# Kernel tuning notes

Measured on AMD Instinct MI355X. Metric: run time of the kernel, lower is better.

Reference implementation:

```python
import jax, jax.numpy as jnp
import numpy as np

B, N, D, K, H = 64, 4096, 256, 15, 512
EPS = 1e-8
LN_EPS = 1e-5

def layer_norm(x, w, b):
    m = jnp.mean(x, axis=-1, keepdims=True)
    v = jnp.mean((x - m) ** 2, axis=-1, keepdims=True)
    return (x - m) / jnp.sqrt(v + LN_EPS) * w + b

def gru_cell(x, h, w_ih, w_hh, b_ih, b_hh):
    gi = x @ w_ih.T + b_ih
    gh = h @ w_hh.T + b_hh
    ir, iz, inn = jnp.split(gi, 3, axis=-1)
    hr, hz, hn = jnp.split(gh, 3, axis=-1)
    r = jax.nn.sigmoid(ir + hr)
    z = jax.nn.sigmoid(iz + hz)
    n = jnp.tanh(inn + r * hn)
    return (1.0 - z) * n + z * h

def setup_inputs() -> dict:
    key = jax.random.key(0)
    ks = jax.random.split(key, 16)
    s = 1.0 / np.sqrt(D)
    return {
        "inputs": jax.random.normal(ks[0], (B, N, D), jnp.float32),
        "slot_noise": jax.random.normal(ks[1], (B, K, D), jnp.float32),
        "slots_mu": jax.random.normal(ks[2], (1, K, D), jnp.float32) * s,
        "slots_logsigma": jnp.zeros((1, K, D), jnp.float32),
        "Wq": jax.random.normal(ks[3], (D, D), jnp.float32) * s,
        "Wk": jax.random.normal(ks[4], (D, D), jnp.float32) * s,
        "Wv": jax.random.normal(ks[5], (D, D), jnp.float32) * s,
        "gru_w_ih": jax.random.normal(ks[6], (3 * D, D), jnp.float32) * s,
        "gru_w_hh": jax.random.normal(ks[7], (3 * D, D), jnp.float32) * s,
        "gru_b_ih": jnp.zeros((3 * D,), jnp.float32),
        "gru_b_hh": jnp.zeros((3 * D,), jnp.float32),
        "mlp_w1": jax.random.normal(ks[8], (H, D), jnp.float32) * s,
        "mlp_b1": jnp.zeros((H,), jnp.float32),
        "mlp_w2": jax.random.normal(ks[9], (D, H), jnp.float32) / np.sqrt(H),
        "mlp_b2": jnp.zeros((D,), jnp.float32),
        "ln_in_w": jnp.ones((D,), jnp.float32), "ln_in_b": jnp.zeros((D,), jnp.float32),
        "ln_slots_w": jnp.ones((D,), jnp.float32), "ln_slots_b": jnp.zeros((D,), jnp.float32),
        "ln_mlp_w": jnp.ones((D,), jnp.float32), "ln_mlp_b": jnp.zeros((D,), jnp.float32),
    }

def reference(inputs, slot_noise, slots_mu, slots_logsigma, Wq, Wk, Wv,
              gru_w_ih, gru_w_hh, gru_b_ih, gru_b_hh,
              mlp_w1, mlp_b1, mlp_w2, mlp_b2,
              ln_in_w, ln_in_b, ln_slots_w, ln_slots_b, ln_mlp_w, ln_mlp_b):
    scale = D ** (-0.5)
    slots = slots_mu + jnp.exp(slots_logsigma) * slot_noise  # (B,K,D)
    x = layer_norm(inputs, ln_in_w, ln_in_b)
    k = x @ Wk.T  # (B,N,D)
    v = x @ Wv.T
    for _ in range(3):
        slots_prev = slots
        s = layer_norm(slots, ln_slots_w, ln_slots_b)
        q = s @ Wq.T  # (B,K,D)
        attn_logits = jnp.einsum('bkd,bnd->bkn', q, k) * scale
        attn = jax.nn.softmax(attn_logits, axis=1)  # softmax over slots
        attn_norm = attn / (jnp.sum(attn, axis=-1, keepdims=True) + EPS)
        updates = jnp.einsum('bkn,bnd->bkd', attn_norm, v)
        slots = gru_cell(updates.reshape(-1, D), slots_prev.reshape(-1, D),
                         gru_w_ih, gru_w_hh, gru_b_ih, gru_b_hh).reshape(B, K, D)
        h1 = jax.nn.relu(layer_norm(slots, ln_mlp_w, ln_mlp_b) @ mlp_w1.T + mlp_b1)
        slots = slots + h1 @ mlp_w2.T + mlp_b2
    s = layer_norm(slots, ln_slots_w, ln_slots_b)
    q = s @ Wq.T
    attn_logits = jnp.einsum('bkd,bnd->bkn', q, k) * scale
    attn = jax.nn.softmax(attn_logits, axis=1)
    return (slots, attn)
```

## Files before the change

### kernel.cpp

```cpp
#include <hip/hip_runtime.h>
#include <hip/hip_bf16.h>
#include <stdint.h>

#define Bh 64
#define Nn 4096
#define Dd 256
#define Kk 15
#define Hh 512
#define BN (Bh*Nn)
#define EPSN 1e-8f
#define LN_EPS 1e-5f

typedef __attribute__((ext_vector_type(8))) short short8;
typedef __attribute__((ext_vector_type(4))) float f32x4;

__device__ __forceinline__ float bflo(unsigned u){ return __uint_as_float(u << 16); }
__device__ __forceinline__ float bfhi(unsigned u){ return __uint_as_float(u & 0xffff0000u); }
__device__ __forceinline__ unsigned short f2bf(float f){
    unsigned b = __float_as_uint(f);
    b += 0x7fffu + ((b >> 16) & 1u);
    return (unsigned short)(b >> 16);
}
__device__ __forceinline__ float sigm_(float x){ return 1.f/(1.f+__expf(-x)); }
__device__ __forceinline__ float tanh_(float x){ return 1.f - 2.f/(__expf(2.f*x)+1.f); }

__device__ __forceinline__ void async16(const void* g, void* l){
    __builtin_amdgcn_global_load_lds((const __attribute__((address_space(1))) void*)g,
                                     (__attribute__((address_space(3))) void*)l, 16, 0, 0);
}

#define OFF_X    ((size_t)0)
#define OFF_K    (OFF_X  + (size_t)BN*256*2)
#define OFF_VT   (OFF_K  + (size_t)BN*256*2)
#define OFF_WC   (OFF_VT + (size_t)BN*256*2)
#define OFF_QBF  (OFF_WC + (size_t)512*256*2)
#define OFF_S    (OFF_QBF+ (size_t)64*16*256*2)
#define OFF_G    (OFF_S  + (size_t)983040)
#define OFF_SN   (OFF_G  + (size_t)983040)
#define OFF_UPD  (OFF_SN + (size_t)983040)
#define OFF_ASUM (OFF_UPD+ (size_t)983040)
#define OFF_GT   (OFF_ASUM+(size_t)4096)
#define OFF_H1   (OFF_GT + (size_t)960*1536*4)

__global__ __launch_bounds__(256) void k_prep_wc(const float* __restrict__ Wk, const float* __restrict__ Wv,
                                                 unsigned short* __restrict__ Wc){
    int i = blockIdx.x*256 + threadIdx.x;
    int n = i >> 8, e = i & 255;
    float w = (n < 256) ? Wk[n*256+e] : Wv[(n-256)*256+e];
    Wc[i] = f2bf(w);
}

__global__ __launch_bounds__(256) void k_slots_init(const float* __restrict__ mu, const float* __restrict__ lsig,
                                                    const float* __restrict__ noise, float* __restrict__ S){
    int i = blockIdx.x*256 + threadIdx.x;
    int j = i % (Kk*Dd);
    S[i] = mu[j] + __expf(lsig[j]) * noise[i];
}

__global__ __launch_bounds__(256) void k_ln_in(const float* __restrict__ x, const float* __restrict__ g,
                                               const float* __restrict__ b, unsigned short* __restrict__ out){
    int wave = threadIdx.x >> 6, lane = threadIdx.x & 63;
    size_t row = (size_t)blockIdx.x*4 + wave;
    const float4* xr = (const float4*)(x + row*Dd);
    float4 v = xr[lane];
    float s  = v.x+v.y+v.z+v.w;
    float ss = v.x*v.x+v.y*v.y+v.z*v.z+v.w*v.w;
    for (int m=1;m<64;m<<=1){ s += __shfl_xor(s,m); ss += __shfl_xor(ss,m); }
    float mean = s*(1.f/Dd);
    float rstd = rsqrtf(ss*(1.f/Dd) - mean*mean + LN_EPS);
    float4 gv = ((const float4*)g)[lane], bv = ((const float4*)b)[lane];
    ushort4 o;
    o.x = f2bf((v.x-mean)*rstd*gv.x + bv.x);
    o.y = f2bf((v.y-mean)*rstd*gv.y + bv.y);
    o.z = f2bf((v.z-mean)*rstd*gv.z + bv.z);
    o.w = f2bf((v.w-mean)*rstd*gv.w + bv.w);
    *(ushort4*)(out + row*Dd + lane*4) = o;
}

__global__ __launch_bounds__(256) void k_ln_rows(const float* __restrict__ x, const float* __restrict__ g,
                                                 const float* __restrict__ b, float* __restrict__ out){
    int wave = threadIdx.x >> 6, lane = threadIdx.x & 63;
    size_t row = (size_t)blockIdx.x*4 + wave;
    const float4* xr = (const float4*)(x + row*Dd);
    float4 v = xr[lane];
    float s  = v.x+v.y+v.z+v.w;
    float ss = v.x*v.x+v.y*v.y+v.z*v.z+v.w*v.w;
    for (int m=1;m<64;m<<=1){ s += __shfl_xor(s,m); ss += __shfl_xor(ss,m); }
    float mean = s*(1.f/Dd);
    float rstd = rsqrtf(ss*(1.f/Dd) - mean*mean + LN_EPS);
    float4 gv = ((const float4*)g)[lane], bv = ((const float4*)b)[lane];
    float4 o;
    o.x = (v.x-mean)*rstd*gv.x + bv.x;
    o.y = (v.y-mean)*rstd*gv.y + bv.y;
    o.z = (v.z-mean)*rstd*gv.z + bv.z;
    o.w = (v.w-mean)*rstd*gv.w + bv.w;
    *(float4*)(out + row*Dd + lane*4) = o;
}

__global__ __launch_bounds__(512, 2) void k_proj(const unsigned short* __restrict__ A,
                                                 const unsigned short* __restrict__ Bw,
                                                 unsigned short* __restrict__ kb,
                                                 unsigned short* __restrict__ vT){
    __shared__ short As[128*256];
    int tid = threadIdx.x;
    int w = tid >> 6, lane = tid & 63;
    int m0 = blockIdx.x*128;
    int wr = w >> 2, wc = w & 3;
    int lr = lane & 15, lg = lane >> 4;

#pragma unroll
    for (int j=0;j<8;j++){
        int idx = j*512 + tid;
        int row = idx >> 5, chp = idx & 31;
        int ch  = chp ^ (row & 7);
        async16((const char*)A + ((size_t)(m0+row)*256 + ch*8)*2, (char*)As + (size_t)idx*16);
    }

    const unsigned short* bwl = Bw + (size_t)(wc*32 + lr)*256 + lg*8;

    short8 A_0,A_1,A_2,A_3, B_0,B_1,B_2,B_3, C_0,C_1,C_2,C_3;
    f32x4 acc00,acc01,acc10,acc11,acc20,acc21,acc30,acc31;

#define ISSUE(P, t_) { \
    const unsigned short* bp_ = bwl + ((t_)>>2)*32768 + (((t_)>>1)&1)*128 + ((t_)&1)*64; \
    P##0 = *(const short8*)(bp_); \
    P##1 = *(const short8*)(bp_ + 32); \
    P##2 = *(const short8*)(bp_ + 4096); \
    P##3 = *(const short8*)(bp_ + 4096 + 32); }
#define LDA(mi_, ks_) (*(const short8*)((const char*)As + (wr*64 + (mi_)*16 + lr)*512 + ((((ks_)*4+lg))^swz)*16))
#define MF(a_,b_,c_) __builtin_amdgcn_mfma_f32_16x16x32_bf16(a_,b_,c_,0,0,0)
#define COMPQ(F0, F1, ks_) { \
    short8 af0=LDA(0,ks_), af1=LDA(1,ks_), af2=LDA(2,ks_), af3=LDA(3,ks_); \
    acc00=MF(af0,F0,acc00); acc01=MF(af0,F1,acc01); \
    acc10=MF(af1,F0,acc10); acc11=MF(af1,F1,acc11); \
    acc20=MF(af2,F0,acc20); acc21=MF(af2,F1,acc21); \
    acc30=MF(af3,F0,acc30); acc31=MF(af3,F1,acc31); }
#define COMPU(P, t_) { COMPQ(P##0, P##2, ((((t_)>>1)&1)*4 + ((t_)&1)*2 + 0)); \
                       COMPQ(P##1, P##3, ((((t_)>>1)&1)*4 + ((t_)&1)*2 + 1)); }
#define ZERO { acc00=acc01=acc10=acc11=acc20=acc21=acc30=acc31=(f32x4){0.f,0.f,0.f,0.f}; }
#define STK(nt_, mi_, ni_, A_) { \
    int gn_ = (nt_)*128 + wc*32 + (ni_)*16 + cn; \
    _Pragma("unroll") for (int r=0;r<4;r++){ \
        size_t gm_ = (size_t)m0 + wr*64 + (mi_)*16 + cr + r; \
        kb[gm_*256 + gn_] = f2bf(A_[r]); } }
#define STV(nt_, mi_, ni_, A_) { \
    int nl_ = nl0 + wr*64 + (mi_)*16 + cr; \
    int d_  = ((nt_)-2)*128 + wc*32 + (ni_)*16 + cn; \
    ushort4 o_; o_.x=f2bf(A_[0]); o_.y=f2bf(A_[1]); o_.z=f2bf(A_[2]); o_.w=f2bf(A_[3]); \
    *(ushort4*)(vT + ((size_t)bb*256 + d_)*4096 + nl_) = o_; }
#define EPI_K(nt_) { STK(nt_,0,0,acc00) STK(nt_,0,1,acc01) STK(nt_,1,0,acc10) STK(nt_,1,1,acc11) \
                     STK(nt_,2,0,acc20) STK(nt_,2,1,acc21) STK(nt_,3,0,acc30) STK(nt_,3,1,acc31) }
#define EPI_V(nt_) { STV(nt_,0,0,acc00) STV(nt_,0,1,acc01) STV(nt_,1,0,acc10) STV(nt_,1,1,acc11) \
                     STV(nt_,2,0,acc20) STV(nt_,2,1,acc21) STV(nt_,3,0,acc30) STV(nt_,3,1,acc31) }

    ISSUE(A_,0) ISSUE(B_,1) ISSUE(C_,2)
    __syncthreads();

    int bb  = m0 >> 12;
    int nl0 = m0 & 4095;
    int cn = lr, cr = lg*4;
    int swz = lr & 7;

    ZERO
    COMPU(A_,0)  ISSUE(A_,3)
    COMPU(B_,1)  ISSUE(B_,4)
    COMPU(C_,2)  ISSUE(C_,5)
    COMPU(A_,3)  ISSUE(A_,6)
    EPI_K(0) ZERO
    COMPU(B_,4)  ISSUE(B_,7)
    COMPU(C_,5)  ISSUE(C_,8)
    COMPU(A_,6)  ISSUE(A_,9)
    COMPU(B_,7)  ISSUE(B_,10)
    EPI_K(1) ZERO
    COMPU(C_,8)  ISSUE(C_,11)
    COMPU(A_,9)  ISSUE(A_,12)
    COMPU(B_,10) ISSUE(B_,13)
    COMPU(C_,11) ISSUE(C_,14)
    EPI_V(2) ZERO
    COMPU(A_,12) ISSUE(A_,15)
    COMPU(B_,13)
    COMPU(C_,14)
    COMPU(A_,15)
    EPI_V(3)

#undef ISSUE
#undef LDA
#undef MF
#undef COMPQ
#undef COMPU
#undef ZERO
#undef STK
#undef STV
#undef EPI_K
#undef EPI_V
}

__global__ __launch_bounds__(256) void k_q(const float* __restrict__ sn, const float* __restrict__ Wq,
                                           unsigned short* __restrict__ qbf){
    int b = blockIdx.x, c = threadIdx.x;
    const float4* wr = (const float4*)(Wq + (size_t)c*256);
    const float4* s4 = (const float4*)(sn + (size_t)b*Kk*Dd);
    float acc[15];
#pragma unroll
    for (int r=0;r<15;r++) acc[r] = 0.f;
    for (int e=0;e<64;e++){
        float4 wv = wr[e];
#pragma unroll
        for (int r=0;r<15;r++){
            float4 sv = s4[r*64+e];
            acc[r] += sv.x*wv.x + sv.y*wv.y + sv.z*wv.z + sv.w*wv.w;
        }
    }
#pragma unroll
    for (int r=0;r<15;r++) qbf[(size_t)b*4096 + r*256 + c] = f2bf(acc[r]);
    qbf[(size_t)b*4096 + 15*256 + c] = 0;
}

__global__ __launch_bounds__(256) void k_attn(const unsigned short* __restrict__ kbuf,
                                              const unsigned short* __restrict__ vT,
                                              const unsigned short* __restrict__ qbf,
                                              float* __restrict__ part, float* __restrict__ asum){
    __shared__ unsigned short qls[16*264];
    __shared__ unsigned short atn[4][16*72];
    __shared__ float asl[16];
    int tid = threadIdx.x;
    int w = tid >> 6, l = tid & 63;
    int b = blockIdx.y, n0 = blockIdx.x*256;
    if (tid < 16) asl[tid] = 0.f;
    {
        const short8* qg = (const short8*)(qbf + (size_t)b*4096);
        for (int i = tid; i < 512; i += 256){
            int row = i >> 5, cc = i & 31;
            *(short8*)&qls[row*264 + cc*8] = qg[i];
        }
    }
    __syncthreads();
    int lr = l & 15, lg = l >> 4;
    f32x4 acc[4];
#pragma unroll
    for (int t=0;t<4;t++) acc[t] = (f32x4){0.f,0.f,0.f,0.f};
    const unsigned short* kb = kbuf + ((size_t)(b*Nn) + n0 + w*64)*256;
#pragma unroll
    for (int ks=0; ks<8; ks++){
        short8 af = *(const short8*)&qls[lr*264 + ks*32 + lg*8];
#pragma unroll
        for (int t=0;t<4;t++){
            short8 bf = *(const short8*)(kb + ((size_t)(t*16+lr))*256 + ks*32 + lg*8);
            acc[t] = __builtin_amdgcn_mfma_f32_16x16x32_bf16(af, bf, acc[t], 0,0,0);
        }
    }
    float asr[4] = {0.f,0.f,0.f,0.f};
#pragma unroll
    for (int t=0;t<4;t++){
        float v0=acc[t][0], v1=acc[t][1], v2=acc[t][2], v3=acc[t][3];
        if (lg==3) v3 = -1e30f;
        float m = fmaxf(fmaxf(v0,v1), fmaxf(v2,v3));
        m = fmaxf(m, __shfl_xor(m,16));
        m = fmaxf(m, __shfl_xor(m,32));
        float e0=__expf((v0-m)*0.0625f), e1=__expf((v1-m)*0.0625f),
              e2=__expf((v2-m)*0.0625f), e3=(lg==3)?0.f:__expf((v3-m)*0.0625f);
        float s = e0+e1+e2+e3;
        s += __shfl_xor(s,16); s += __shfl_xor(s,32);
        float inv = 1.f/s;
        e0*=inv; e1*=inv; e2*=inv; e3*=inv;
        unsigned short* a_ = &atn[w][0];
        int col = t*16 + lr;
        a_[(lg*4+0)*72+col] = f2bf(e0);
        a_[(lg*4+1)*72+col] = f2bf(e1);
        a_[(lg*4+2)*72+col] = f2bf(e2);
        a_[(lg*4+3)*72+col] = f2bf(e3);
        float p0=e0,p1=e1,p2=e2,p3=e3;
        for (int mk=1;mk<16;mk<<=1){
            p0+=__shfl_xor(p0,mk); p1+=__shfl_xor(p1,mk);
            p2+=__shfl_xor(p2,mk); p3+=__shfl_xor(p3,mk);
        }
        asr[0]+=p0; asr[1]+=p1; asr[2]+=p2; asr[3]+=p3;
    }
    if (lr == 0){
        atomicAdd(&asl[lg*4+0], asr[0]);
        atomicAdd(&asl[lg*4+1], asr[1]);
        atomicAdd(&asl[lg*4+2], asr[2]);
        atomicAdd(&asl[lg*4+3], asr[3]);
    }
    __syncthreads();
    f32x4 ua[4];
#pragma unroll
    for (int dt=0;dt<4;dt++) ua[dt] = (f32x4){0.f,0.f,0.f,0.f};
    const unsigned short* vb = vT + (size_t)b*256*4096 + ((size_t)(w*64 + lr))*4096 + n0 + lg*8;
#pragma unroll
    for (int wn=0;wn<4;wn++)
#pragma unroll
        for (int kc=0;kc<2;kc++){
            short8 af = *(const short8*)&atn[wn][lr*72 + kc*32 + lg*8];
#pragma unroll
            for (int dt=0;dt<4;dt++){
                short8 bf = *(const short8*)(vb + (size_t)dt*16*4096 + wn*64 + kc*32);
                ua[dt] = __builtin_amdgcn_mfma_f32_16x16x32_bf16(af, bf, ua[dt], 0,0,0);
            }
        }
    float* pb = part + ((size_t)(b*16 + blockIdx.x))*4096;
#pragma unroll
    for (int dt=0;dt<4;dt++)
#pragma unroll
        for (int r=0;r<4;r++)
            pb[(lg*4+r)*256 + w*64 + dt*16 + lr] = ua[dt][r];
    if (tid < 15) atomicAdd(&asum[b*15+tid], asl[tid]);
}

__global__ __launch_bounds__(256) void k_upd_reduce(const float* __restrict__ part, float* __restrict__ upd){
    int i = blockIdx.x*256 + threadIdx.x;
    int b = i / 3840, rem = i - b*3840;
    const float* p = part + (size_t)b*16*4096 + rem;
    float s = 0.f;
#pragma unroll
    for (int j=0;j<16;j++) s += p[j*4096];
    upd[i] = s;
}

__global__ __launch_bounds__(256) void k_gates(const float* __restrict__ upd, const float* __restrict__ asum,
                                               const float* __restrict__ S,
                                               const float* __restrict__ wih, const float* __restrict__ whh,
                                               const float* __restrict__ bih, const float* __restrict__ bhh,
                                               float* __restrict__ gates){
    int b = blockIdx.y;
    int c = blockIdx.x*256 + threadIdx.x;
    bool isGI = (c < 768);
    const float* wrow = isGI ? (wih + (size_t)c*256) : (whh + (size_t)(c-768)*256);
    const float* src  = isGI ? (upd + (size_t)b*Kk*Dd) : (S + (size_t)b*Kk*Dd);
    float bias = isGI ? bih[c] : bhh[c-768];
    const float4* w4 = (const float4*)wrow;
    const float4* s4 = (const float4*)src;
    float acc[15];
#pragma unroll
    for (int r=0;r<15;r++) acc[r] = 0.f;
    for (int e=0;e<64;e++){
        float4 wv = w4[e];
#pragma unroll
        for (int r=0;r<15;r++){
            float4 sv = s4[r*64+e];
            acc[r] += sv.x*wv.x + sv.y*wv.y + sv.z*wv.z + sv.w*wv.w;
        }
    }
#pragma unroll
    for (int r=0;r<15;r++){
        float v = acc[r];
        if (isGI) v *= 1.f/(asum[b*Kk+r] + EPSN);
        gates[((size_t)(b*Kk+r))*1536 + c] = v + bias;
    }
}

__global__ __launch_bounds__(256) void k_gru(const float* __restrict__ gates, const float* __restrict__ S,
                                             float* __restrict__ G){
    int row = blockIdx.x, d = threadIdx.x;
    const float* gr = gates + (size_t)row*1536;
    float ir=gr[d], iz=gr[256+d], inn=gr[512+d];
    float hr=gr[768+d], hz=gr[1024+d], hn=gr[1280+d];
    float r = sigm_(ir+hr), z = sigm_(iz+hz);
    float n = tanh_(inn + r*hn);
    float h = S[(size_t)row*Dd + d];
    G[(size_t)row*Dd + d] = (1.f-z)*n + z*h;
}

__global__ __launch_bounds__(256) void k_mlp1(const float* __restrict__ sn, const float* __restrict__ w1,
                                              const float* __restrict__ b1, float* __restrict__ h1){
    int b = blockIdx.y;
    int c = blockIdx.x*256 + threadIdx.x;
    const float4* w4 = (const float4*)(w1 + (size_t)c*256);
    const float4* s4 = (const float4*)(sn + (size_t)b*Kk*Dd);
    float acc[15];
#pragma unroll
    for (int r=0;r<15;r++) acc[r] = 0.f;
    for (int e=0;e<64;e++){
        float4 wv = w4[e];
#pragma unroll
        for (int r=0;r<15;r++){
            float4 sv = s4[r*64+e];
            acc[r] += sv.x*wv.x + sv.y*wv.y + sv.z*wv.z + sv.w*wv.w;
        }
    }
    float bias = b1[c];
#pragma unroll
    for (int r=0;r<15;r++)
        h1[((size_t)(b*Kk+r))*Hh + c] = fmaxf(acc[r] + bias, 0.f);
}

__global__ __launch_bounds__(256) void k_mlp2(const float* __restrict__ G, const float* __restrict__ h1,
                                              const float* __restrict__ w2, const float* __restrict__ b2,
                                              float* __restrict__ S){
    int b = blockIdx.x, c = threadIdx.x;
    const float4* w4 = (const float4*)(w2 + (size_t)c*512);
    const float4* h4 = (const float4*)(h1 + (size_t)b*Kk*Hh);
    float acc[15];
#pragma unroll
    for (int r=0;r<15;r++) acc[r] = 0.f;
    for (int e=0;e<128;e++){
        float4 wv = w4[e];
#pragma unroll
        for (int r=0;r<15;r++){
            float4 hv = h4[r*128+e];
            acc[r] += hv.x*wv.x + hv.y*wv.y + hv.z*wv.z + hv.w*wv.w;
        }
    }
    float bias = b2[c];
#pragma unroll
    for (int r=0;r<15;r++){
        size_t i = ((size_t)(b*Kk+r))*Dd + c;
        S[i] = G[i] + acc[r] + bias;
    }
}

__global__ __launch_bounds__(256) void k_attn_out(const unsigned short* __restrict__ kbuf,
                                                  const unsigned short* __restrict__ qbf,
                                                  float* __restrict__ out){
    __shared__ unsigned short qls[16*264];
    int tid = threadIdx.x;
    int w = tid >> 6, l = tid & 63;
    int b = blockIdx.y, n0 = blockIdx.x*256;
    {
        const short8* qg = (const short8*)(qbf + (size_t)b*4096);
        for (int i = tid; i < 512; i += 256){
            int row = i >> 5, cc = i & 31;
            *(short8*)&qls[row*264 + cc*8] = qg[i];
        }
    }
    __syncthreads();
    int lr = l & 15, lg = l >> 4;
    f32x4 acc[4];
#pragma unroll
    for (int t=0;t<4;t++) acc[t] = (f32x4){0.f,0.f,0.f,0.f};
    const unsigned short* kb = kbuf + ((size_t)(b*Nn) + n0 + w*64)*256;
#pragma unroll
    for (int ks=0; ks<8; ks++){
        short8 af = *(const short8*)&qls[lr*264 + ks*32 + lg*8];
#pragma unroll
        for (int t=0;t<4;t++){
            short8 bf = *(const short8*)(kb + ((size_t)(t*16+lr))*256 + ks*32 + lg*8);
            acc[t] = __builtin_amdgcn_mfma_f32_16x16x32_bf16(af, bf, acc[t], 0,0,0);
        }
    }
#pragma unroll
    for (int t=0;t<4;t++){
        float v0=acc[t][0], v1=acc[t][1], v2=acc[t][2], v3=acc[t][3];
        if (lg==3) v3 = -1e30f;
        float m = fmaxf(fmaxf(v0,v1), fmaxf(v2,v3));
        m = fmaxf(m, __shfl_xor(m,16));
        m = fmaxf(m, __shfl_xor(m,32));
        float e0=__expf((v0-m)*0.0625f), e1=__expf((v1-m)*0.0625f),
              e2=__expf((v2-m)*0.0625f), e3=(lg==3)?0.f:__expf((v3-m)*0.0625f);
        float s = e0+e1+e2+e3;
        s += __shfl_xor(s,16); s += __shfl_xor(s,32);
        float inv = 1.f/s;
        int n = n0 + w*64 + t*16 + lr;
        float ee0=e0*inv, ee1=e1*inv, ee2=e2*inv, ee3=e3*inv;
        out[((size_t)(b*15 + lg*4+0))*4096 + n] = ee0;
        out[((size_t)(b*15 + lg*4+1))*4096 + n] = ee1;
        out[((size_t)(b*15 + lg*4+2))*4096 + n] = ee2;
        if (lg != 3) out[((size_t)(b*15 + lg*4+3))*4096 + n] = ee3;
    }
}

__global__ __launch_bounds__(256) void k_copy(const float* __restrict__ src, float* __restrict__ dst){
    int i = blockIdx.x*256 + threadIdx.x;
    dst[i] = src[i];
}

extern "C" void kernel_launch(void* const* d_in, const int* in_sizes, int n_in,
                              void* d_out, int out_size, void* d_ws, size_t ws_size,
                              hipStream_t stream) {
    const float* inputs = (const float*)d_in[0];
    const float* noise  = (const float*)d_in[1];
    const float* mu     = (const float*)d_in[2];
    const float* lsig   = (const float*)d_in[3];
    const float* Wq     = (const float*)d_in[4];
    const float* Wk     = (const float*)d_in[5];
    const float* Wv     = (const float*)d_in[6];
    const float* wih    = (const float*)d_in[7];
    const float* whh    = (const float*)d_in[8];
    const float* bih    = (const float*)d_in[9];
    const float* bhh    = (const float*)d_in[10];
    const float* w1     = (const float*)d_in[11];
    const float* b1     = (const float*)d_in[12];
    const float* w2     = (const float*)d_in[13];
    const float* b2     = (const float*)d_in[14];
    const float* lin_w  = (const float*)d_in[15];
    const float* lin_b  = (const float*)d_in[16];
    const float* lsl_w  = (const float*)d_in[17];
    const float* lsl_b  = (const float*)d_in[18];
    const float* lml_w  = (const float*)d_in[19];
    const float* lml_b  = (const float*)d_in[20];

    char* ws = (char*)d_ws;
    unsigned short* xbf  = (unsigned short*)(ws + OFF_X);
    float*          PART = (float*)(ws + OFF_X);
    unsigned short* kbuf = (unsigned short*)(ws + OFF_K);
    unsigned short* vT   = (unsigned short*)(ws + OFF_VT);
    unsigned short* wc   = (unsigned short*)(ws + OFF_WC);
    unsigned short* QBF  = (unsigned short*)(ws + OFF_QBF);
    float* S    = (float*)(ws + OFF_S);
    float* G    = (float*)(ws + OFF_G);
    float* SN   = (float*)(ws + OFF_SN);
    float* UPD  = (float*)(ws + OFF_UPD);
    float* ASUM = (float*)(ws + OFF_ASUM);
    float* GT   = (float*)(ws + OFF_GT);
    float* H1   = (float*)(ws + OFF_H1);
    float* out  = (float*)d_out;

    k_prep_wc<<<512, 256, 0, stream>>>(Wk, Wv, wc);
    k_slots_init<<<960, 256, 0, stream>>>(mu, lsig, noise, S);
    k_ln_in<<<BN/4, 256, 0, stream>>>(inputs, lin_w, lin_b, xbf);
    k_proj<<<BN/128, 512, 0, stream>>>(xbf, wc, kbuf, vT);

    for (int it = 0; it < 3; it++){
        k_ln_rows<<<240, 256, 0, stream>>>(S, lsl_w, lsl_b, SN);
        k_q<<<Bh, 256, 0, stream>>>(SN, Wq, QBF);
        hipMemsetAsync(ASUM, 0, 4096, stream);
        k_attn<<<dim3(16, Bh), 256, 0, stream>>>(kbuf, vT, QBF, PART, ASUM);
        k_upd_reduce<<<960, 256, 0, stream>>>(PART, UPD);
        k_gates<<<dim3(6, Bh), 256, 0, stream>>>(UPD, ASUM, S, wih, whh, bih, bhh, GT);
        k_gru<<<960, 256, 0, stream>>>(GT, S, G);
        k_ln_rows<<<240, 256, 0, stream>>>(G, lml_w, lml_b, SN);
        k_mlp1<<<dim3(2, Bh), 256, 0, stream>>>(SN, w1, b1, H1);
        k_mlp2<<<Bh, 256, 0, stream>>>(G, H1, w2, b2, S);
    }

    k_ln_rows<<<240, 256, 0, stream>>>(S, lsl_w, lsl_b, SN);
    k_q<<<Bh, 256, 0, stream>>>(SN, Wq, QBF);
    k_attn_out<<<dim3(16, Bh), 256, 0, stream>>>(kbuf, QBF, out + 245760);
    k_copy<<<960, 256, 0, stream>>>(S, out);
}
```

Before: 1.407 ms.

## Fuse layer norms into consumer kernels and fold reductions into gate kernel

Fuses the input layer norm into the K/V projection kernel, which now reads fp32 inputs and writes normalized bf16 rows straight into LDS, so the bf16 x intermediate is never written to or read from global memory. Slot and MLP layer norms move into the q and mlp1 kernels. Attention partial sums and row sums are reduced inside the gates kernel instead of through an atomic memset path and a separate reduce kernel. The final slots are written to the output from mlp2, which removes the copy kernel. The projection kernel loses its async global-to-LDS loads and does more ALU work before the MFMA phase, and each gates block repeats the partial reduction.

```diff
diff --git a/kernel.cpp b/kernel.cpp
--- a/kernel.cpp
+++ b/kernel.cpp
@@ -14,8 +14,6 @@
 typedef __attribute__((ext_vector_type(8))) short short8;
 typedef __attribute__((ext_vector_type(4))) float f32x4;
 
-__device__ __forceinline__ float bflo(unsigned u){ return __uint_as_float(u << 16); }
-__device__ __forceinline__ float bfhi(unsigned u){ return __uint_as_float(u & 0xffff0000u); }
 __device__ __forceinline__ unsigned short f2bf(float f){
     unsigned b = __float_as_uint(f);
     b += 0x7fffu + ((b >> 16) & 1u);
@@ -23,11 +21,6 @@
 }
 __device__ __forceinline__ float sigm_(float x){ return 1.f/(1.f+__expf(-x)); }
 __device__ __forceinline__ float tanh_(float x){ return 1.f - 2.f/(__expf(2.f*x)+1.f); }
-
-__device__ __forceinline__ void async16(const void* g, void* l){
-    __builtin_amdgcn_global_load_lds((const __attribute__((address_space(1))) void*)g,
-                                     (__attribute__((address_space(3))) void*)l, 16, 0, 0);
-}
 
 #define OFF_X    ((size_t)0)
 #define OFF_K    (OFF_X  + (size_t)BN*256*2)
@@ -57,47 +50,9 @@
     S[i] = mu[j] + __expf(lsig[j]) * noise[i];
 }
 
-__global__ __launch_bounds__(256) void k_ln_in(const float* __restrict__ x, const float* __restrict__ g,
-                                               const float* __restrict__ b, unsigned short* __restrict__ out){
-    int wave = threadIdx.x >> 6, lane = threadIdx.x & 63;
-    size_t row = (size_t)blockIdx.x*4 + wave;
-    const float4* xr = (const float4*)(x + row*Dd);
-    float4 v = xr[lane];
-    float s  = v.x+v.y+v.z+v.w;
-    float ss = v.x*v.x+v.y*v.y+v.z*v.z+v.w*v.w;
-    for (int m=1;m<64;m<<=1){ s += __shfl_xor(s,m); ss += __shfl_xor(ss,m); }
-    float mean = s*(1.f/Dd);
-    float rstd = rsqrtf(ss*(1.f/Dd) - mean*mean + LN_EPS);
-    float4 gv = ((const float4*)g)[lane], bv = ((const float4*)b)[lane];
-    ushort4 o;
-    o.x = f2bf((v.x-mean)*rstd*gv.x + bv.x);
-    o.y = f2bf((v.y-mean)*rstd*gv.y + bv.y);
-    o.z = f2bf((v.z-mean)*rstd*gv.z + bv.z);
-    o.w = f2bf((v.w-mean)*rstd*gv.w + bv.w);
-    *(ushort4*)(out + row*Dd + lane*4) = o;
-}
-
-__global__ __launch_bounds__(256) void k_ln_rows(const float* __restrict__ x, const float* __restrict__ g,
-                                                 const float* __restrict__ b, float* __restrict__ out){
-    int wave = threadIdx.x >> 6, lane = threadIdx.x & 63;
-    size_t row = (size_t)blockIdx.x*4 + wave;
-    const float4* xr = (const float4*)(x + row*Dd);
-    float4 v = xr[lane];
-    float s  = v.x+v.y+v.z+v.w;
-    float ss = v.x*v.x+v.y*v.y+v.z*v.z+v.w*v.w;
-    for (int m=1;m<64;m<<=1){ s += __shfl_xor(s,m); ss += __shfl_xor(ss,m); }
-    float mean = s*(1.f/Dd);
-    float rstd = rsqrtf(ss*(1.f/Dd) - mean*mean + LN_EPS);
-    float4 gv = ((const float4*)g)[lane], bv = ((const float4*)b)[lane];
-    float4 o;
-    o.x = (v.x-mean)*rstd*gv.x + bv.x;
-    o.y = (v.y-mean)*rstd*gv.y + bv.y;
-    o.z = (v.z-mean)*rstd*gv.z + bv.z;
-    o.w = (v.w-mean)*rstd*gv.w + bv.w;
-    *(float4*)(out + row*Dd + lane*4) = o;
-}
-
-__global__ __launch_bounds__(512, 2) void k_proj(const unsigned short* __restrict__ A,
+__global__ __launch_bounds__(512, 2) void k_proj(const float* __restrict__ X,
+                                                 const float* __restrict__ lnw,
+                                                 const float* __restrict__ lnb,
                                                  const unsigned short* __restrict__ Bw,
                                                  unsigned short* __restrict__ kb,
                                                  unsigned short* __restrict__ vT){
@@ -108,12 +63,32 @@
     int wr = w >> 2, wc = w & 3;
     int lr = lane & 15, lg = lane >> 4;
 
-#pragma unroll
-    for (int j=0;j<8;j++){
-        int idx = j*512 + tid;
-        int row = idx >> 5, chp = idx & 31;
-        int ch  = chp ^ (row & 7);
-        async16((const char*)A + ((size_t)(m0+row)*256 + ch*8)*2, (char*)As + (size_t)idx*16);
+    {
+        float4 gv = ((const float4*)lnw)[lane];
+        float4 bv = ((const float4*)lnb)[lane];
+        const float* xr0 = X + ((size_t)(m0 + w*16))*256 + lane*4;
+#pragma unroll
+        for (int bt=0; bt<2; bt++){
+            float4 xv[8];
+#pragma unroll
+            for (int r=0;r<8;r++) xv[r] = *(const float4*)(xr0 + (size_t)(bt*8+r)*256);
+#pragma unroll
+            for (int r=0;r<8;r++){
+                float4 v = xv[r];
+                float s  = v.x+v.y+v.z+v.w;
+                float ss = v.x*v.x+v.y*v.y+v.z*v.z+v.w*v.w;
+                for (int mk=1;mk<64;mk<<=1){ s += __shfl_xor(s,mk); ss += __shfl_xor(ss,mk); }
+                float mean = s*(1.f/256.f);
+                float rstd = rsqrtf(ss*(1.f/256.f) - mean*mean + LN_EPS);
+                ushort4 o;
+                o.x = f2bf((v.x-mean)*rstd*gv.x + bv.x);
+                o.y = f2bf((v.y-mean)*rstd*gv.y + bv.y);
+                o.z = f2bf((v.z-mean)*rstd*gv.z + bv.z);
+                o.w = f2bf((v.w-mean)*rstd*gv.w + bv.w);
+                int row = w*16 + bt*8 + r;
+                *(ushort4*)((char*)As + row*512 + (((lane>>1)^(row&7))<<4) + ((lane&1)<<3)) = o;
+            }
+        }
     }
 
     const unsigned short* bwl = Bw + (size_t)(wc*32 + lr)*256 + lg*8;
@@ -195,31 +170,53 @@
 #undef EPI_V
 }
 
-__global__ __launch_bounds__(256) void k_q(const float* __restrict__ sn, const float* __restrict__ Wq,
-                                           unsigned short* __restrict__ qbf){
-    int b = blockIdx.x, c = threadIdx.x;
-    const float4* wr = (const float4*)(Wq + (size_t)c*256);
-    const float4* s4 = (const float4*)(sn + (size_t)b*Kk*Dd);
+__global__ __launch_bounds__(256) void k_lnq(const float* __restrict__ S,
+                                             const float* __restrict__ g, const float* __restrict__ b,
+                                             const float* __restrict__ Wq,
+                                             unsigned short* __restrict__ qbf){
+    __shared__ float sn[15*256];
+    int tid = threadIdx.x, w = tid >> 6, lane = tid & 63;
+    int bb = blockIdx.x;
+    {
+        float4 gv = ((const float4*)g)[lane], bv = ((const float4*)b)[lane];
+        for (int r=w; r<15; r+=4){
+            float4 v = *(const float4*)(S + ((size_t)bb*15 + r)*256 + lane*4);
+            float s  = v.x+v.y+v.z+v.w;
+            float ss = v.x*v.x+v.y*v.y+v.z*v.z+v.w*v.w;
+            for (int mk=1;mk<64;mk<<=1){ s += __shfl_xor(s,mk); ss += __shfl_xor(ss,mk); }
+            float mean = s*(1.f/256.f);
+            float rstd = rsqrtf(ss*(1.f/256.f) - mean*mean + LN_EPS);
+            float4 o;
+            o.x = (v.x-mean)*rstd*gv.x + bv.x;
+            o.y = (v.y-mean)*rstd*gv.y + bv.y;
+            o.z = (v.z-mean)*rstd*gv.z + bv.z;
+            o.w = (v.w-mean)*rstd*gv.w + bv.w;
+            *(float4*)(sn + r*256 + lane*4) = o;
+        }
+    }
+    __syncthreads();
+    int c = tid;
+    const float4* wr4 = (const float4*)(Wq + (size_t)c*256);
     float acc[15];
 #pragma unroll
     for (int r=0;r<15;r++) acc[r] = 0.f;
     for (int e=0;e<64;e++){
-        float4 wv = wr[e];
+        float4 wv = wr4[e];
 #pragma unroll
         for (int r=0;r<15;r++){
-            float4 sv = s4[r*64+e];
+            float4 sv = *(const float4*)(sn + r*256 + e*4);
             acc[r] += sv.x*wv.x + sv.y*wv.y + sv.z*wv.z + sv.w*wv.w;
         }
     }
 #pragma unroll
-    for (int r=0;r<15;r++) qbf[(size_t)b*4096 + r*256 + c] = f2bf(acc[r]);
-    qbf[(size_t)b*4096 + 15*256 + c] = 0;
+    for (int r=0;r<15;r++) qbf[(size_t)bb*4096 + r*256 + c] = f2bf(acc[r]);
+    qbf[(size_t)bb*4096 + 15*256 + c] = 0;
 }
 
 __global__ __launch_bounds__(256) void k_attn(const unsigned short* __restrict__ kbuf,
                                               const unsigned short* __restrict__ vT,
                                               const unsigned short* __restrict__ qbf,
-                                              float* __restrict__ part, float* __restrict__ asum){
+                                              float* __restrict__ part, float* __restrict__ asump){
     __shared__ unsigned short qls[16*264];
     __shared__ unsigned short atn[4][16*72];
     __shared__ float asl[16];
@@ -304,32 +301,45 @@
 #pragma unroll
         for (int r=0;r<4;r++)
             pb[(lg*4+r)*256 + w*64 + dt*16 + lr] = ua[dt][r];
-    if (tid < 15) atomicAdd(&asum[b*15+tid], asl[tid]);
-}
-
-__global__ __launch_bounds__(256) void k_upd_reduce(const float* __restrict__ part, float* __restrict__ upd){
-    int i = blockIdx.x*256 + threadIdx.x;
-    int b = i / 3840, rem = i - b*3840;
-    const float* p = part + (size_t)b*16*4096 + rem;
-    float s = 0.f;
-#pragma unroll
-    for (int j=0;j<16;j++) s += p[j*4096];
-    upd[i] = s;
-}
-
-__global__ __launch_bounds__(256) void k_gates(const float* __restrict__ upd, const float* __restrict__ asum,
+    if (tid < 15) asump[((size_t)(b*16 + blockIdx.x))*16 + tid] = asl[tid];
+}
+
+__global__ __launch_bounds__(256) void k_gates(const float* __restrict__ part,
+                                               const float* __restrict__ asump,
                                                const float* __restrict__ S,
                                                const float* __restrict__ wih, const float* __restrict__ whh,
                                                const float* __restrict__ bih, const float* __restrict__ bhh,
                                                float* __restrict__ gates){
-    int b = blockIdx.y;
-    int c = blockIdx.x*256 + threadIdx.x;
-    bool isGI = (c < 768);
+    __shared__ float src[3840];
+    __shared__ float asl[15];
+    int b = blockIdx.y, x = blockIdx.x, tid = threadIdx.x;
+    int c = x*256 + tid;
+    bool isGI = (x < 3);
+    if (isGI){
+        const float4* p0 = (const float4*)(part + (size_t)b*16*4096);
+        for (int i=tid; i<960; i+=256){
+            float4 s = p0[i];
+#pragma unroll
+            for (int j=1;j<16;j++){
+                float4 t = p0[j*1024 + i];
+                s.x+=t.x; s.y+=t.y; s.z+=t.z; s.w+=t.w;
+            }
+            ((float4*)src)[i] = s;
+        }
+        if (tid < 15){
+            float a = 0.f;
+#pragma unroll
+            for (int j=0;j<16;j++) a += asump[((size_t)b*16 + j)*16 + tid];
+            asl[tid] = a;
+        }
+    } else {
+        const float4* s0 = (const float4*)(S + (size_t)b*3840);
+        for (int i=tid; i<960; i+=256) ((float4*)src)[i] = s0[i];
+    }
+    __syncthreads();
     const float* wrow = isGI ? (wih + (size_t)c*256) : (whh + (size_t)(c-768)*256);
-    const float* src  = isGI ? (upd + (size_t)b*Kk*Dd) : (S + (size_t)b*Kk*Dd);
     float bias = isGI ? bih[c] : bhh[c-768];
     const float4* w4 = (const float4*)wrow;
-    const float4* s4 = (const float4*)src;
     float acc[15];
 #pragma unroll
     for (int r=0;r<15;r++) acc[r] = 0.f;
@@ -337,15 +347,15 @@
         float4 wv = w4[e];
 #pragma unroll
         for (int r=0;r<15;r++){
-            float4 sv = s4[r*64+e];
+            float4 sv = *(const float4*)(src + r*256 + e*4);
             acc[r] += sv.x*wv.x + sv.y*wv.y + sv.z*wv.z + sv.w*wv.w;
         }
     }
 #pragma unroll
     for (int r=0;r<15;r++){
         float v = acc[r];
-        if (isGI) v *= 1.f/(asum[b*Kk+r] + EPSN);
-        gates[((size_t)(b*Kk+r))*1536 + c] = v + bias;
+        if (isGI) v *= 1.f/(asl[r] + EPSN);
+        gates[((size_t)(b*15+r))*1536 + c] = v + bias;
     }
 }
 
@@ -361,12 +371,33 @@
     G[(size_t)row*Dd + d] = (1.f-z)*n + z*h;
 }
 
-__global__ __launch_bounds__(256) void k_mlp1(const float* __restrict__ sn, const float* __restrict__ w1,
-                                              const float* __restrict__ b1, float* __restrict__ h1){
-    int b = blockIdx.y;
-    int c = blockIdx.x*256 + threadIdx.x;
+__global__ __launch_bounds__(256) void k_lnmlp1(const float* __restrict__ G,
+                                                const float* __restrict__ g, const float* __restrict__ b,
+                                                const float* __restrict__ w1, const float* __restrict__ b1,
+                                                float* __restrict__ h1){
+    __shared__ float sn[15*256];
+    int tid = threadIdx.x, w = tid >> 6, lane = tid & 63;
+    int bb = blockIdx.y;
+    {
+        float4 gv = ((const float4*)g)[lane], bv = ((const float4*)b)[lane];
+        for (int r=w; r<15; r+=4){
+            float4 v = *(const float4*)(G + ((size_t)bb*15 + r)*256 + lane*4);
+            float s  = v.x+v.y+v.z+v.w;
+            float ss = v.x*v.x+v.y*v.y+v.z*v.z+v.w*v.w;
+            for (int mk=1;mk<64;mk<<=1){ s += __shfl_xor(s,mk); ss += __shfl_xor(ss,mk); }
+            float mean = s*(1.f/256.f);
+            float rstd = rsqrtf(ss*(1.f/256.f) - mean*mean + LN_EPS);
+            float4 o;
+            o.x = (v.x-mean)*rstd*gv.x + bv.x;
+            o.y = (v.y-mean)*rstd*gv.y + bv.y;
+            o.z = (v.z-mean)*rstd*gv.z + bv.z;
+            o.w = (v.w-mean)*rstd*gv.w + bv.w;
+            *(float4*)(sn + r*256 + lane*4) = o;
+        }
+    }
+    __syncthreads();
+    int c = blockIdx.x*256 + tid;
     const float4* w4 = (const float4*)(w1 + (size_t)c*256);
-    const float4* s4 = (const float4*)(sn + (size_t)b*Kk*Dd);
     float acc[15];
 #pragma unroll
     for (int r=0;r<15;r++) acc[r] = 0.f;
@@ -374,19 +405,19 @@
         float4 wv = w4[e];
 #pragma unroll
         for (int r=0;r<15;r++){
-            float4 sv = s4[r*64+e];
+            float4 sv = *(const float4*)(sn + r*256 + e*4);
             acc[r] += sv.x*wv.x + sv.y*wv.y + sv.z*wv.z + sv.w*wv.w;
         }
     }
     float bias = b1[c];
 #pragma unroll
     for (int r=0;r<15;r++)
-        h1[((size_t)(b*Kk+r))*Hh + c] = fmaxf(acc[r] + bias, 0.f);
+        h1[((size_t)(bb*15+r))*Hh + c] = fmaxf(acc[r] + bias, 0.f);
 }
 
 __global__ __launch_bounds__(256) void k_mlp2(const float* __restrict__ G, const float* __restrict__ h1,
                                               const float* __restrict__ w2, const float* __restrict__ b2,
-                                              float* __restrict__ S){
+                                              float* __restrict__ S, float* __restrict__ dup){
     int b = blockIdx.x, c = threadIdx.x;
     const float4* w4 = (const float4*)(w2 + (size_t)c*512);
     const float4* h4 = (const float4*)(h1 + (size_t)b*Kk*Hh);
@@ -405,7 +436,9 @@
 #pragma unroll
     for (int r=0;r<15;r++){
         size_t i = ((size_t)(b*Kk+r))*Dd + c;
-        S[i] = G[i] + acc[r] + bias;
+        float val = G[i] + acc[r] + bias;
+        S[i] = val;
+        if (dup) dup[i] = val;
     }
 }
 
@@ -457,11 +490,6 @@
         out[((size_t)(b*15 + lg*4+2))*4096 + n] = ee2;
         if (lg != 3) out[((size_t)(b*15 + lg*4+3))*4096 + n] = ee3;
     }
-}
-
-__global__ __launch_bounds__(256) void k_copy(const float* __restrict__ src, float* __restrict__ dst){
-    int i = blockIdx.x*256 + threadIdx.x;
-    dst[i] = src[i];
 }
 
 extern "C" void kernel_launch(void* const* d_in, const int* in_sizes, int n_in,
@@ -490,41 +518,31 @@
     const float* lml_b  = (const float*)d_in[20];
 
     char* ws = (char*)d_ws;
-    unsigned short* xbf  = (unsigned short*)(ws + OFF_X);
     float*          PART = (float*)(ws + OFF_X);
     unsigned short* kbuf = (unsigned short*)(ws + OFF_K);
     unsigned short* vT   = (unsigned short*)(ws + OFF_VT);
     unsigned short* wc   = (unsigned short*)(ws + OFF_WC);
     unsigned short* QBF  = (unsigned short*)(ws + OFF_QBF);
-    float* S    = (float*)(ws + OFF_S);
-    float* G    = (float*)(ws + OFF_G);
-    float* SN   = (float*)(ws + OFF_SN);
-    float* UPD  = (float*)(ws + OFF_UPD);
-    float* ASUM = (float*)(ws + OFF_ASUM);
-    float* GT   = (float*)(ws + OFF_GT);
-    float* H1   = (float*)(ws + OFF_H1);
-    float* out  = (float*)d_out;
+    float* S     = (float*)(ws + OFF_S);
+    float* G     = (float*)(ws + OFF_G);
+    float* ASUMP = (float*)(ws + OFF_UPD);
+    float* GT    = (float*)(ws + OFF_GT);
+    float* H1    = (float*)(ws + OFF_H1);
+    float* out   = (float*)d_out;
 
     k_prep_wc<<<512, 256, 0, stream>>>(Wk, Wv, wc);
     k_slots_init<<<960, 256, 0, stream>>>(mu, lsig, noise, S);
-    k_ln_in<<<BN/4, 256, 0, stream>>>(inputs, lin_w, lin_b, xbf);
-    k_proj<<<BN/128, 512, 0, stream>>>(xbf, wc, kbuf, vT);
+    k_proj<<<BN/128, 512, 0, stream>>>(inputs, lin_w, lin_b, wc, kbuf, vT);
 
     for (int it = 0; it < 3; it++){
-        k_ln_rows<<<240, 256, 0, stream>>>(S, lsl_w, lsl_b, SN);
-        k_q<<<Bh, 256, 0, stream>>>(SN, Wq, QBF);
-        hipMemsetAsync(ASUM, 0, 4096, stream);
-        k_attn<<<dim3(16, Bh), 256, 0, stream>>>(kbuf, vT, QBF, PART, ASUM);
-        k_upd_reduce<<<960, 256, 0, stream>>>(PART, UPD);
-        k_gates<<<dim3(6, Bh), 256, 0, stream>>>(UPD, ASUM, S, wih, whh, bih, bhh, GT);
+        k_lnq<<<Bh, 256, 0, stream>>>(S, lsl_w, lsl_b, Wq, QBF);
+        k_attn<<<dim3(16, Bh), 256, 0, stream>>>(kbuf, vT, QBF, PART, ASUMP);
+        k_gates<<<dim3(6, Bh), 256, 0, stream>>>(PART, ASUMP, S, wih, whh, bih, bhh, GT);
         k_gru<<<960, 256, 0, stream>>>(GT, S, G);
-        k_ln_rows<<<240, 256, 0, stream>>>(G, lml_w, lml_b, SN);
-        k_mlp1<<<dim3(2, Bh), 256, 0, stream>>>(SN, w1, b1, H1);
-        k_mlp2<<<Bh, 256, 0, stream>>>(G, H1, w2, b2, S);
-    }
-
-    k_ln_rows<<<240, 256, 0, stream>>>(S, lsl_w, lsl_b, SN);
-    k_q<<<Bh, 256, 0, stream>>>(SN, Wq, QBF);
+        k_lnmlp1<<<dim3(2, Bh), 256, 0, stream>>>(G, lml_w, lml_b, w1, b1, H1);
+        k_mlp2<<<Bh, 256, 0, stream>>>(G, H1, w2, b2, S, (it==2) ? out : (float*)nullptr);
+    }
+
+    k_lnq<<<Bh, 256, 0, stream>>>(S, lsl_w, lsl_b, Wq, QBF);
     k_attn_out<<<dim3(16, Bh), 256, 0, stream>>>(kbuf, QBF, out + 245760);
-    k_copy<<<960, 256, 0, stream>>>(S, out);
-}
+}
```

Result: faster. 1.280 ms (-9.0%).
